# Kernel tuning notes

Hardware: AMD Instinct MI355X
Metric: run time of the kernel (lower is better)

The kernel has to match this reference:

```python
import jax, jax.numpy as jnp
import numpy as np

B, C, L, F = 4096, 1000, 32, 64


def _l2norm(x, eps=1e-12):
    # torch F.normalize: x / max(||x||_2, eps)
    n = jnp.sqrt(jnp.sum(x * x, axis=-1, keepdims=True))
    return x / jnp.maximum(n, eps)


def setup_inputs() -> dict:
    key = jax.random.key(0)
    k1, k2, k3 = jax.random.split(key, 3)
    pe = jax.random.normal(k1, (B, L, F), dtype=jnp.float32)
    cm = jax.random.uniform(k2, (B,), dtype=jnp.float32)
    class_signatures = jax.random.normal(k3, (C, L, F), dtype=jnp.float32) * 0.1
    cantor_prototypes = jnp.linspace(0.0, 1.0, C, dtype=jnp.float32)
    level_resonance = jnp.ones((C, L), dtype=jnp.float32) / L
    return {
        "pe_levels": pe,
        "cantor_measures": cm,
        "class_signatures": class_signatures,
        "cantor_prototypes": cantor_prototypes,
        "level_resonance": level_resonance,
    }


def reference(pe_levels, cantor_measures, class_signatures, cantor_prototypes, level_resonance):
    eps = 1e-6
    # --- triadic compatibility ---
    pe_norm = _l2norm(pe_levels)                     # [B,L,F]
    sig_norm = _l2norm(class_signatures)             # [C,L,F]
    sims = jnp.einsum('blf,clf->bcl', pe_norm, sig_norm)
    sims = (sims + 1.0) * 0.5                        # [B,C,L]
    resonance = jax.nn.softmax(level_resonance, axis=-1)  # [C,L]
    triadic = jnp.sum(sims * resonance[None, :, :], axis=-1)  # [B,C]
    # --- self-similarity pattern (vectorized over level pairs) ---
    a = pe_levels[:, :-1, :]                         # [B,L-1,F]
    b = pe_levels[:, 1:, :]
    cos_eps = 1e-8
    dot = jnp.sum(a * b, axis=-1)
    na = jnp.maximum(jnp.sqrt(jnp.sum(a * a, axis=-1)), cos_eps)
    nb = jnp.maximum(jnp.sqrt(jnp.sum(b * b, axis=-1)), cos_eps)
    self_sim = (dot / (na * nb) + 1.0) * 0.5         # [B,L-1]
    expected = jax.nn.sigmoid(level_resonance[:, :-1] - level_resonance[:, 1:])  # [C,L-1]
    pattern_diff = jnp.abs(self_sim[:, None, :] - expected[None, :, :])  # [B,C,L-1]
    self_sim_compat = jnp.clip(1.0 - jnp.mean(pattern_diff, axis=-1), 0.0, 1.0)  # [B,C]
    # --- cantor compatibility ---
    d = jnp.abs(cantor_measures[:, None] - cantor_prototypes[None, :])
    cantor_compat = jnp.exp(-(d * d) / 0.1) + 1e-8   # [B,C]
    # --- hierarchical compatibility ---
    split = L // 2
    early = _l2norm(jnp.mean(pe_levels[:, :split, :], axis=1))          # [B,F]
    late = _l2norm(jnp.mean(pe_levels[:, split:, :], axis=1))
    early_t = _l2norm(jnp.mean(class_signatures[:, :split, :], axis=1))  # [C,F]
    late_t = _l2norm(jnp.mean(class_signatures[:, split:, :], axis=1))
    early_c = (early @ early_t.T + 1.0) * 0.5
    late_c = (late @ late_t.T + 1.0) * 0.5
    hier = (early_c + late_c) * 0.5                  # [B,C]
    # --- geometric mean of four clamped terms ---
    t = jnp.clip(triadic, eps, 1.0)
    s = jnp.clip(self_sim_compat, eps, 1.0)
    c = jnp.clip(cantor_compat, eps, 1.0)
    h = jnp.clip(hier, eps, 1.0)
    return (t * s * c * h) ** 0.25
```

## Files before the change

### kernel.cpp

```cpp
#include <hip/hip_runtime.h>
#include <hip/hip_bf16.h>

typedef float f32x4 __attribute__((ext_vector_type(4)));
typedef short bf16x8 __attribute__((ext_vector_type(8)));

#define B_DIM 4096
#define C_DIM 1000
#define CP 1024
#define K1 2048
#define EPS 1e-6f

__device__ __forceinline__ float wsum(float v) {
#pragma unroll
  for (int o = 32; o > 0; o >>= 1) v += __shfl_xor(v, o, 64);
  return v;
}
__device__ __forceinline__ float wmax(float v) {
#pragma unroll
  for (int o = 32; o > 0; o >>= 1) v = fmaxf(v, __shfl_xor(v, o, 64));
  return v;
}

__device__ __forceinline__ void load_lds16(const void* g, void* l) {
  __builtin_amdgcn_global_load_lds(
      (const __attribute__((address_space(1))) unsigned int*)g,
      (__attribute__((address_space(3))) unsigned int*)l, 16, 0, 0);
}

__global__ void prep_all(const float* __restrict__ sig,
                         const float* __restrict__ lr,
                         const float* __restrict__ pe,
                         __hip_bfloat16* __restrict__ wsig,
                         float* __restrict__ expd,
                         __hip_bfloat16* __restrict__ elc,
                         __hip_bfloat16* __restrict__ pen,
                         float* __restrict__ ssb,
                         __hip_bfloat16* __restrict__ elb) {
  __shared__ float LW[4][2304];
  __shared__ float AUX[4][32];
  const int w = threadIdx.x >> 6;
  const int t = threadIdx.x & 63;
  const int unit = blockIdx.x * 4 + w;
  const bool isClass = unit < CP;
  const int c = unit;
  const int b = unit - CP;
  const bool pad = isClass && (c >= C_DIM);
  const float* src = isClass ? (sig + (size_t)c * K1) : (pe + (size_t)b * K1);

#pragma unroll
  for (int i = 0; i < 8; ++i) {
    int o = i * 256 + t * 4;
    f32x4 v = {0.f, 0.f, 0.f, 0.f};
    if (!pad) v = *(const f32x4*)(src + o);
    *(f32x4*)&LW[w][(o >> 6) * 72 + (o & 63)] = v;
  }
  __syncthreads();

  if (isClass) {
    float lv = (t < 32 && !pad) ? lr[c * 32 + t] : -3.0e38f;
    float mx = wmax(lv);
    float ev = (t < 32 && !pad) ? expf(lv - mx) : 0.f;
    float sden = wsum(ev);
    float res = pad ? 0.f : ev / sden;
    float lvn = __shfl_down(lv, 1, 64);
    if (t < 31) {
      expd[c * 32 + t] = pad ? 0.f : 1.f / (1.f + expf(-(lv - lvn)));
    } else if (t == 31) {
      expd[c * 32 + 31] = 0.f;
    }
    if (t < 32) {
      f32x4 sq = {0.f, 0.f, 0.f, 0.f};
#pragma unroll
      for (int i = 0; i < 16; ++i) {
        f32x4 v = *(const f32x4*)&LW[w][t * 72 + i * 4];
        sq += v * v;
      }
      float s = sq[0] + sq[1] + sq[2] + sq[3];
      float inv = 1.f / fmaxf(sqrtf(s), 1e-12f);
      AUX[w][t] = inv * res;
    }
  } else {
    if (t < 32) {
      f32x4 sq = {0.f, 0.f, 0.f, 0.f}, dt = {0.f, 0.f, 0.f, 0.f};
      const int tn = (t < 31) ? t + 1 : t;
#pragma unroll
      for (int i = 0; i < 16; ++i) {
        f32x4 v = *(const f32x4*)&LW[w][t * 72 + i * 4];
        f32x4 vn = *(const f32x4*)&LW[w][tn * 72 + i * 4];
        sq += v * v;
        dt += v * vn;
      }
      float s = sq[0] + sq[1] + sq[2] + sq[3];
      float d = dt[0] + dt[1] + dt[2] + dt[3];
      float nrm = sqrtf(s);
      AUX[w][t] = 1.f / fmaxf(nrm, 1e-12f);
      float nn = __shfl_down(nrm, 1, 64);
      if (t < 31)
        ssb[(size_t)b * 32 + t] =
            (d / (fmaxf(nrm, 1e-8f) * fmaxf(nn, 1e-8f)) + 1.f) * 0.5f;
      else
        ssb[(size_t)b * 32 + 31] = 0.f;
    }
  }
  __syncthreads();

  __hip_bfloat16* dst = isClass ? (wsig + (size_t)c * K1) : (pen + (size_t)b * K1);
  float es = 0.f, ls = 0.f;
#pragma unroll
  for (int l = 0; l < 32; ++l) {
    float v = LW[w][l * 72 + t];
    float m = AUX[w][l];
    dst[l * 64 + t] = __float2bfloat16(v * m);
    if (l < 16) es += v; else ls += v;
  }
  es *= (1.f / 16.f);
  ls *= (1.f / 16.f);
  float en = fmaxf(sqrtf(wsum(es * es)), 1e-12f);
  float ln2 = fmaxf(sqrtf(wsum(ls * ls)), 1e-12f);
  __hip_bfloat16* el = isClass ? (elc + (size_t)c * 128) : (elb + (size_t)b * 128);
  el[t] = __float2bfloat16(es / en);
  el[64 + t] = __float2bfloat16(ls / ln2);
}

__global__ __launch_bounds__(512, 2)
void basin_main(const __hip_bfloat16* __restrict__ pen,
                const __hip_bfloat16* __restrict__ wsig,
                const __hip_bfloat16* __restrict__ elb,
                const __hip_bfloat16* __restrict__ elc,
                const float* __restrict__ ssb,
                const float* __restrict__ expd,
                const float* __restrict__ cm,
                const float* __restrict__ proto,
                float* __restrict__ out) {
  __shared__ __align__(16) char smem[131072];
  const int t = threadIdx.x;
  const int lane = t & 63;
  const int w = t >> 6;
  const int wm = w >> 2, wn = w & 3;
  const int brow = blockIdx.x * 128;
  const int bcol = blockIdx.y * 128;
  const int srow8 = t >> 3;
  const int sel8 = (((t & 7) ^ (srow8 & 7)) << 3);
  const int l15 = lane & 15;
  const int gq = lane >> 4;

  const int rowA = (wm * 64 + l15) << 7;
  const int rowB = (wn * 32 + l15) << 7;
  int xg[2];
#pragma unroll
  for (int kk = 0; kk < 2; ++kk) xg[kk] = (((kk * 4 + gq) ^ (l15 & 7)) << 4);

  f32x4 acc1[4][2] = {};
  f32x4 acc2[4][2] = {};

#define STAGE_T(kt, BI)                                                                   \
  do {                                                                                    \
    _Pragma("unroll") for (int i = 0; i < 2; ++i) {                                       \
      load_lds16(pen + (size_t)(brow + i * 64 + srow8) * K1 + (kt) * 64 + sel8,           \
                 smem + (BI) * 32768 + i * 8192 + t * 16);                                \
      load_lds16(wsig + (size_t)(bcol + i * 64 + srow8) * K1 + (kt) * 64 + sel8,          \
                 smem + (BI) * 32768 + 16384 + i * 8192 + t * 16);                        \
    }                                                                                     \
  } while (0)

#define STAGE_H(s, BI)                                                                    \
  do {                                                                                    \
    _Pragma("unroll") for (int i = 0; i < 2; ++i) {                                       \
      load_lds16(elb + (size_t)(brow + i * 64 + srow8) * 128 + (s) * 64 + sel8,           \
                 smem + (BI) * 32768 + i * 8192 + t * 16);                                \
      load_lds16(elc + (size_t)(bcol + i * 64 + srow8) * 128 + (s) * 64 + sel8,           \
                 smem + (BI) * 32768 + 16384 + i * 8192 + t * 16);                        \
    }                                                                                     \
  } while (0)

#define COMPUTE(ACC, BI)                                                                  \
  do {                                                                                    \
    _Pragma("unroll") for (int kk = 0; kk < 2; ++kk) {                                    \
      bf16x8 af[4], bg[2];                                                                \
      _Pragma("unroll") for (int m = 0; m < 4; ++m)                                       \
          af[m] = *(const bf16x8*)(smem + (BI) * 32768 + rowA + m * 2048 + xg[kk]);       \
      _Pragma("unroll") for (int n = 0; n < 2; ++n)                                       \
          bg[n] = *(const bf16x8*)(smem + (BI) * 32768 + 16384 + rowB + n * 2048 + xg[kk]); \
      _Pragma("unroll") for (int m = 0; m < 4; ++m)                                       \
        _Pragma("unroll") for (int n = 0; n < 2; ++n)                                     \
          ACC[m][n] = __builtin_amdgcn_mfma_f32_16x16x32_bf16(af[m], bg[n], ACC[m][n], 0, 0, 0); \
    }                                                                                     \
  } while (0)

#define VMW(N) asm volatile("s_waitcnt vmcnt(" #N ")" ::: "memory")
#define BAR()                    \
  __builtin_amdgcn_s_barrier();  \
  __builtin_amdgcn_sched_barrier(0)

#define KSTEP_S(kt, BI, NXT)                                                              \
  do {                                                                                    \
    VMW(8);                                                                               \
    BAR();                                                                                \
    STAGE_T((kt) + 3, NXT);                                                               \
    COMPUTE(acc1, BI);                                                                    \
  } while (0)

  STAGE_T(0, 0);
  STAGE_T(1, 1);
  STAGE_T(2, 2);
  for (int kt = 0; kt < 28; kt += 4) {
    KSTEP_S(kt, 0, 3);
    KSTEP_S(kt + 1, 1, 0);
    KSTEP_S(kt + 2, 2, 1);
    KSTEP_S(kt + 3, 3, 2);
  }
  VMW(8); BAR(); STAGE_T(31, 3); COMPUTE(acc1, 0);
  VMW(8); BAR(); COMPUTE(acc1, 1);
  VMW(4); BAR(); COMPUTE(acc1, 2);
  VMW(0); BAR(); COMPUTE(acc1, 3);

  STAGE_H(0, 0);
  STAGE_H(1, 1);
  VMW(4); BAR();
  COMPUTE(acc2, 0);
  VMW(0); BAR();
  COMPUTE(acc2, 1);
  __syncthreads();

  float* ss_l = (float*)smem;
  float* ex_l = (float*)(smem + 18432);
  float* cm_l = (float*)(smem + 36864);
  float* pr_l = (float*)(smem + 37376);
  for (int i = t; i < 4096; i += 512) {
    int r = i >> 5, l = i & 31;
    ss_l[r * 36 + l] = ssb[(size_t)(brow + r) * 32 + l];
    ex_l[r * 36 + l] = expd[(size_t)(bcol + r) * 32 + l];
  }
  if (t < 128) cm_l[t] = cm[brow + t];
  else if (t < 256) pr_l[t - 128] = (bcol + t - 128 < C_DIM) ? proto[bcol + t - 128] : 0.f;
  __syncthreads();

  const int col0 = wn * 32 + l15;
  const int row0 = wm * 64 + (gq << 2);
#pragma unroll
  for (int m = 0; m < 4; ++m) {
    float ssum[4][2];
#pragma unroll
    for (int j = 0; j < 4; ++j)
#pragma unroll
      for (int n = 0; n < 2; ++n) ssum[j][n] = 0.f;
#pragma unroll
    for (int l4 = 0; l4 < 32; l4 += 4) {
      f32x4 evv[2], sv[4];
#pragma unroll
      for (int n = 0; n < 2; ++n)
        evv[n] = *(const f32x4*)&ex_l[(col0 + n * 16) * 36 + l4];
#pragma unroll
      for (int j = 0; j < 4; ++j)
        sv[j] = *(const f32x4*)&ss_l[(row0 + m * 16 + j) * 36 + l4];
#pragma unroll
      for (int j = 0; j < 4; ++j)
#pragma unroll
        for (int n = 0; n < 2; ++n) {
          ssum[j][n] += fabsf(sv[j][0] - evv[n][0]) + fabsf(sv[j][1] - evv[n][1]) +
                        fabsf(sv[j][2] - evv[n][2]) + fabsf(sv[j][3] - evv[n][3]);
        }
    }
#pragma unroll
    for (int j = 0; j < 4; ++j) {
      int rloc = row0 + m * 16 + j;
      float cmv = cm_l[rloc];
#pragma unroll
      for (int n = 0; n < 2; ++n) {
        int cloc = col0 + n * 16;
        int cg = bcol + cloc;
        float tria = fminf(fmaxf(0.5f + 0.5f * acc1[m][n][j], EPS), 1.0f);
        float hier = fminf(fmaxf(0.5f + 0.25f * acc2[m][n][j], EPS), 1.0f);
        float sc = fminf(fmaxf(1.0f - ssum[j][n] * (1.0f / 31.0f), EPS), 1.0f);
        float d = cmv - pr_l[cloc];
        float cc = __expf(d * d * -10.0f) + 1e-8f;
        cc = fminf(fmaxf(cc, EPS), 1.0f);
        float p = tria * sc * cc * hier;
        if (cg < C_DIM)
          out[(size_t)(brow + rloc) * C_DIM + cg] = sqrtf(sqrtf(p));
      }
    }
  }
}

extern "C" void kernel_launch(void* const* d_in, const int* in_sizes, int n_in,
                              void* d_out, int out_size, void* d_ws, size_t ws_size,
                              hipStream_t stream) {
  (void)in_sizes; (void)n_in; (void)out_size; (void)ws_size;
  const float* pe = (const float*)d_in[0];
  const float* cm = (const float*)d_in[1];
  const float* sig = (const float*)d_in[2];
  const float* proto = (const float*)d_in[3];
  const float* lr = (const float*)d_in[4];
  float* out = (float*)d_out;
  char* ws = (char*)d_ws;

  __hip_bfloat16* wsig = (__hip_bfloat16*)(ws);
  __hip_bfloat16* pen = (__hip_bfloat16*)(ws + 4194304);
  __hip_bfloat16* elb = (__hip_bfloat16*)(ws + 20971520);
  __hip_bfloat16* elc = (__hip_bfloat16*)(ws + 22020096);
  float* ssb = (float*)(ws + 22282240);
  float* expd = (float*)(ws + 22806528);

  prep_all<<<(CP + B_DIM) / 4, 256, 0, stream>>>(sig, lr, pe, wsig, expd, elc, pen, ssb, elb);
  dim3 grid(B_DIM / 128, CP / 128);
  basin_main<<<grid, 512, 0, stream>>>(pen, wsig, elb, elc, ssb, expd, cm, proto, out);
}
```

Baseline: 59.10 us.

## Switch triadic GEMM operands from bf16 to fp8 e4m3 with scaled MFMA

Normalized pe and weighted class signatures are now stored as fp8 e4m3 instead of bf16. The class side is prescaled by 32 to keep values in fp8 range, and the epilogue divides that scale back out. The main GEMM uses the 16x16x32 fp8 MFMA with 128-byte K tiles, which halves both the K iterations and the bytes staged per tile. The intent is to halve the memory traffic and the MFMA work, at the cost of precision in the triadic similarity term.

Result: faster. 56.66 us (median of 3 runs) (-4.1%).

```diff
diff --git a/kernel.cpp b/kernel.cpp
--- a/kernel.cpp
+++ b/kernel.cpp
@@ -1,5 +1,6 @@
 #include <hip/hip_runtime.h>
 #include <hip/hip_bf16.h>
+#include <hip/hip_fp8.h>
 
 typedef float f32x4 __attribute__((ext_vector_type(4)));
 typedef short bf16x8 __attribute__((ext_vector_type(8)));
@@ -30,10 +31,10 @@
 __global__ void prep_all(const float* __restrict__ sig,
                          const float* __restrict__ lr,
                          const float* __restrict__ pe,
-                         __hip_bfloat16* __restrict__ wsig,
+                         __hip_fp8_e4m3* __restrict__ wsig,
                          float* __restrict__ expd,
                          __hip_bfloat16* __restrict__ elc,
-                         __hip_bfloat16* __restrict__ pen,
+                         __hip_fp8_e4m3* __restrict__ pen,
                          float* __restrict__ ssb,
                          __hip_bfloat16* __restrict__ elb) {
   __shared__ float LW[4][2304];
@@ -77,7 +78,7 @@
       }
       float s = sq[0] + sq[1] + sq[2] + sq[3];
       float inv = 1.f / fmaxf(sqrtf(s), 1e-12f);
-      AUX[w][t] = inv * res;
+      AUX[w][t] = inv * res * 32.f;
     }
   } else {
     if (t < 32) {
@@ -104,13 +105,13 @@
   }
   __syncthreads();
 
-  __hip_bfloat16* dst = isClass ? (wsig + (size_t)c * K1) : (pen + (size_t)b * K1);
+  __hip_fp8_e4m3* dst = isClass ? (wsig + (size_t)c * K1) : (pen + (size_t)b * K1);
   float es = 0.f, ls = 0.f;
 #pragma unroll
   for (int l = 0; l < 32; ++l) {
     float v = LW[w][l * 72 + t];
     float m = AUX[w][l];
-    dst[l * 64 + t] = __float2bfloat16(v * m);
+    dst[l * 64 + t] = __hip_fp8_e4m3(v * m);
     if (l < 16) es += v; else ls += v;
   }
   es *= (1.f / 16.f);
@@ -123,8 +124,8 @@
 }
 
 __global__ __launch_bounds__(512, 2)
-void basin_main(const __hip_bfloat16* __restrict__ pen,
-                const __hip_bfloat16* __restrict__ wsig,
+void basin_main(const unsigned char* __restrict__ pen,
+                const unsigned char* __restrict__ wsig,
                 const __hip_bfloat16* __restrict__ elb,
                 const __hip_bfloat16* __restrict__ elc,
                 const float* __restrict__ ssb,
@@ -139,16 +140,21 @@
   const int wm = w >> 2, wn = w & 3;
   const int brow = blockIdx.x * 128;
   const int bcol = blockIdx.y * 128;
-  const int srow8 = t >> 3;
-  const int sel8 = (((t & 7) ^ (srow8 & 7)) << 3);
+  const int srow = t >> 3;
+  const int schunk = t & 7;
+  const int sel = ((schunk ^ (srow & 7)) << 4);
   const int l15 = lane & 15;
   const int gq = lane >> 4;
 
   const int rowA = (wm * 64 + l15) << 7;
   const int rowB = (wn * 32 + l15) << 7;
-  int xg[2];
-#pragma unroll
-  for (int kk = 0; kk < 2; ++kk) xg[kk] = (((kk * 4 + gq) ^ (l15 & 7)) << 4);
+  int xg8[4];
+#pragma unroll
+  for (int kk = 0; kk < 4; ++kk)
+    xg8[kk] = ((((kk * 2 + (gq >> 1)) ^ (l15 & 7)) << 4) | ((gq & 1) << 3));
+  int xgh[2];
+#pragma unroll
+  for (int kk = 0; kk < 2; ++kk) xgh[kk] = (((kk * 4 + gq) ^ (l15 & 7)) << 4);
 
   f32x4 acc1[4][2] = {};
   f32x4 acc2[4][2] = {};
@@ -156,9 +162,9 @@
 #define STAGE_T(kt, BI)                                                                   \
   do {                                                                                    \
     _Pragma("unroll") for (int i = 0; i < 2; ++i) {                                       \
-      load_lds16(pen + (size_t)(brow + i * 64 + srow8) * K1 + (kt) * 64 + sel8,           \
+      load_lds16(pen + (size_t)(brow + i * 64 + srow) * K1 + (kt) * 128 + sel,            \
                  smem + (BI) * 32768 + i * 8192 + t * 16);                                \
-      load_lds16(wsig + (size_t)(bcol + i * 64 + srow8) * K1 + (kt) * 64 + sel8,          \
+      load_lds16(wsig + (size_t)(bcol + i * 64 + srow) * K1 + (kt) * 128 + sel,           \
                  smem + (BI) * 32768 + 16384 + i * 8192 + t * 16);                        \
     }                                                                                     \
   } while (0)
@@ -166,21 +172,35 @@
 #define STAGE_H(s, BI)                                                                    \
   do {                                                                                    \
     _Pragma("unroll") for (int i = 0; i < 2; ++i) {                                       \
-      load_lds16(elb + (size_t)(brow + i * 64 + srow8) * 128 + (s) * 64 + sel8,           \
+      load_lds16(elb + (size_t)(brow + i * 64 + srow) * 128 + (s) * 64 + (sel >> 1),      \
                  smem + (BI) * 32768 + i * 8192 + t * 16);                                \
-      load_lds16(elc + (size_t)(bcol + i * 64 + srow8) * 128 + (s) * 64 + sel8,           \
+      load_lds16(elc + (size_t)(bcol + i * 64 + srow) * 128 + (s) * 64 + (sel >> 1),      \
                  smem + (BI) * 32768 + 16384 + i * 8192 + t * 16);                        \
     }                                                                                     \
   } while (0)
 
 #define COMPUTE(ACC, BI)                                                                  \
+  do {                                                                                    \
+    _Pragma("unroll") for (int kk = 0; kk < 4; ++kk) {                                    \
+      long af[4], bg[2];                                                                  \
+      _Pragma("unroll") for (int m = 0; m < 4; ++m)                                       \
+          af[m] = *(const long*)(smem + (BI) * 32768 + rowA + m * 2048 + xg8[kk]);        \
+      _Pragma("unroll") for (int n = 0; n < 2; ++n)                                       \
+          bg[n] = *(const long*)(smem + (BI) * 32768 + 16384 + rowB + n * 2048 + xg8[kk]); \
+      _Pragma("unroll") for (int m = 0; m < 4; ++m)                                       \
+        _Pragma("unroll") for (int n = 0; n < 2; ++n)                                     \
+          ACC[m][n] = __builtin_amdgcn_mfma_f32_16x16x32_fp8_fp8(af[m], bg[n], ACC[m][n], 0, 0, 0); \
+    }                                                                                     \
+  } while (0)
+
+#define COMPUTE_H(ACC, BI)                                                                \
   do {                                                                                    \
     _Pragma("unroll") for (int kk = 0; kk < 2; ++kk) {                                    \
       bf16x8 af[4], bg[2];                                                                \
       _Pragma("unroll") for (int m = 0; m < 4; ++m)                                       \
-          af[m] = *(const bf16x8*)(smem + (BI) * 32768 + rowA + m * 2048 + xg[kk]);       \
+          af[m] = *(const bf16x8*)(smem + (BI) * 32768 + rowA + m * 2048 + xgh[kk]);      \
       _Pragma("unroll") for (int n = 0; n < 2; ++n)                                       \
-          bg[n] = *(const bf16x8*)(smem + (BI) * 32768 + 16384 + rowB + n * 2048 + xg[kk]); \
+          bg[n] = *(const bf16x8*)(smem + (BI) * 32768 + 16384 + rowB + n * 2048 + xgh[kk]); \
       _Pragma("unroll") for (int m = 0; m < 4; ++m)                                       \
         _Pragma("unroll") for (int n = 0; n < 2; ++n)                                     \
           ACC[m][n] = __builtin_amdgcn_mfma_f32_16x16x32_bf16(af[m], bg[n], ACC[m][n], 0, 0, 0); \
@@ -203,13 +223,13 @@
   STAGE_T(0, 0);
   STAGE_T(1, 1);
   STAGE_T(2, 2);
-  for (int kt = 0; kt < 28; kt += 4) {
+  for (int kt = 0; kt < 12; kt += 4) {
     KSTEP_S(kt, 0, 3);
     KSTEP_S(kt + 1, 1, 0);
     KSTEP_S(kt + 2, 2, 1);
     KSTEP_S(kt + 3, 3, 2);
   }
-  VMW(8); BAR(); STAGE_T(31, 3); COMPUTE(acc1, 0);
+  VMW(8); BAR(); STAGE_T(15, 3); COMPUTE(acc1, 0);
   VMW(8); BAR(); COMPUTE(acc1, 1);
   VMW(4); BAR(); COMPUTE(acc1, 2);
   VMW(0); BAR(); COMPUTE(acc1, 3);
@@ -217,9 +237,9 @@
   STAGE_H(0, 0);
   STAGE_H(1, 1);
   VMW(4); BAR();
-  COMPUTE(acc2, 0);
+  COMPUTE_H(acc2, 0);
   VMW(0); BAR();
-  COMPUTE(acc2, 1);
+  COMPUTE_H(acc2, 1);
   __syncthreads();
 
   float* ss_l = (float*)smem;
@@ -269,7 +289,7 @@
       for (int n = 0; n < 2; ++n) {
         int cloc = col0 + n * 16;
         int cg = bcol + cloc;
-        float tria = fminf(fmaxf(0.5f + 0.5f * acc1[m][n][j], EPS), 1.0f);
+        float tria = fminf(fmaxf(0.5f + acc1[m][n][j] * 0.015625f, EPS), 1.0f);
         float hier = fminf(fmaxf(0.5f + 0.25f * acc2[m][n][j], EPS), 1.0f);
         float sc = fminf(fmaxf(1.0f - ssum[j][n] * (1.0f / 31.0f), EPS), 1.0f);
         float d = cmv - pr_l[cloc];
@@ -295,14 +315,15 @@
   float* out = (float*)d_out;
   char* ws = (char*)d_ws;
 
-  __hip_bfloat16* wsig = (__hip_bfloat16*)(ws);
-  __hip_bfloat16* pen = (__hip_bfloat16*)(ws + 4194304);
-  __hip_bfloat16* elb = (__hip_bfloat16*)(ws + 20971520);
-  __hip_bfloat16* elc = (__hip_bfloat16*)(ws + 22020096);
-  float* ssb = (float*)(ws + 22282240);
-  float* expd = (float*)(ws + 22806528);
+  __hip_fp8_e4m3* wsig = (__hip_fp8_e4m3*)(ws);
+  __hip_fp8_e4m3* pen = (__hip_fp8_e4m3*)(ws + 2097152);
+  __hip_bfloat16* elb = (__hip_bfloat16*)(ws + 10485760);
+  __hip_bfloat16* elc = (__hip_bfloat16*)(ws + 11534336);
+  float* ssb = (float*)(ws + 11796480);
+  float* expd = (float*)(ws + 12320768);
 
   prep_all<<<(CP + B_DIM) / 4, 256, 0, stream>>>(sig, lr, pe, wsig, expd, elc, pen, ssb, elb);
   dim3 grid(B_DIM / 128, CP / 128);
-  basin_main<<<grid, 512, 0, stream>>>(pen, wsig, elb, elc, ssb, expd, cm, proto, out);
-}
+  basin_main<<<grid, 512, 0, stream>>>((const unsigned char*)pen, (const unsigned char*)wsig,
+                                       elb, elc, ssb, expd, cm, proto, out);
+}
```
